# Kernel tuning notes

Measured on AMD Instinct MI355X. Metric: run time of the kernel, lower is better.

Reference implementation:

```python
import jax, jax.numpy as jnp
import numpy as np

N_NODES = 20000


def _segment_softmax(alpha, dst, num_nodes):
    # numerically-stable softmax over edges grouped by destination node
    m = jax.ops.segment_max(alpha, dst, num_segments=num_nodes)
    m = jnp.where(jnp.isfinite(m), m, 0.0)
    a = jnp.exp(alpha - m[dst])
    denom = jax.ops.segment_sum(a, dst, num_segments=num_nodes)
    return a / denom[dst]


def mgcn_conv(x, src, dst, edge_type, basis, att, weight, root, bias, num_nodes):
    # x: [N, in], basis: [B, in, out], att: [R, B], weight: [R, out=in]
    x_i = x[dst]                                   # [E, in] target feats
    x_j = x[src]                                   # [E, in] source feats
    # per-edge attention logit: sum_d x_i[d] * w_r[d] * x_j[d]
    alpha = jnp.sum(x_i * weight[edge_type] * x_j, axis=1)   # [E]
    alpha = _segment_softmax(alpha, dst, num_nodes)          # [E]
    # basis-decomposed per-edge transform: x_j @ (att_r . basis)
    t = jnp.einsum('ei,bio->ebo', x_j, basis)                # [E, B, out]
    msg = jnp.einsum('ebo,eb->eo', t, att[edge_type])        # [E, out]
    msg = msg * alpha[:, None]
    out = jax.ops.segment_sum(msg, dst, num_segments=num_nodes)  # [N, out]
    return out + x @ root + bias


def setup_inputs() -> dict:
    key = jax.random.key(0)
    ks = jax.random.split(key, 16)
    E, D, R, B, N = 32768, 128, 474, 64, N_NODES
    s = 0.05
    return {
        'entity': jnp.arange(N, dtype=jnp.int64) if jax.config.jax_enable_x64 else jnp.arange(N, dtype=jnp.int32),
        'edge_index': jax.random.randint(ks[0], (2, E), 0, N, dtype=jnp.int32),
        'edge_type': jax.random.randint(ks[1], (E,), 0, R, dtype=jnp.int32),
        'emb_table': jax.random.normal(ks[2], (N, D), dtype=jnp.float32),
        'basis1': jax.random.normal(ks[3], (B, D, D), dtype=jnp.float32) * s,
        'att1': jax.random.normal(ks[4], (R, B), dtype=jnp.float32) * s,
        'weight1': jax.random.normal(ks[5], (R, D), dtype=jnp.float32) * s,
        'root1': jax.random.normal(ks[6], (D, D), dtype=jnp.float32) * s,
        'bias1': jnp.zeros((D,), dtype=jnp.float32),
        'basis2': jax.random.normal(ks[7], (B, D, D), dtype=jnp.float32) * s,
        'att2': jax.random.normal(ks[8], (R, B), dtype=jnp.float32) * s,
        'weight2': jax.random.normal(ks[9], (R, D), dtype=jnp.float32) * s,
        'root2': jax.random.normal(ks[10], (D, D), dtype=jnp.float32) * s,
        'bias2': jnp.zeros((D,), dtype=jnp.float32),
    }


def reference(entity, edge_index, edge_type, emb_table,
              basis1, att1, weight1, root1, bias1,
              basis2, att2, weight2, root2, bias2):
    src, dst = edge_index[0], edge_index[1]   # PyG: (source j, target i)
    x = emb_table[entity]                     # embedding lookup
    h = jax.nn.relu(mgcn_conv(x, src, dst, edge_type, basis1, att1,
                              weight1, root1, bias1, N_NODES))
    # dropout is identity at inference
    out = mgcn_conv(h, src, dst, edge_type, basis2, att2,
                    weight2, root2, bias2, N_NODES)
    return out
```

## Files before the change

kernel.cpp:

```cpp
#include <hip/hip_runtime.h>
#include <hip/hip_bf16.h>

#define N_NODES 20000
#define N_EDGES 32768
#define DIM 128
#define N_REL 474
#define N_BASIS 64
#define TILE_E 64
#define WSTRIDE 264
#define LELIST 1024

#define WMIX_BLKS 128
#define ROOTT_BLK 1
#define RG1_BASE (WMIX_BLKS + ROOTT_BLK)
#define RG1_BLKS ((N_NODES + 63) / 64)
#define GATHER_BASE (RG1_BASE + RG1_BLKS)
#define PREP_GRID 1024

#define MSG_REL_BLKS (2 * N_REL)
#define MERGE_GRID 1024

typedef __bf16 bf16x8 __attribute__((ext_vector_type(8)));
typedef float f32x4 __attribute__((ext_vector_type(4)));

__device__ __forceinline__ unsigned short f2b(float f) {
    unsigned u = __float_as_uint(f);
    unsigned r = (u + 0x7FFFu + ((u >> 16) & 1u)) >> 16;
    return (unsigned short)r;
}
__device__ __forceinline__ float b2f(unsigned short s) {
    return __uint_as_float(((unsigned)s) << 16);
}
__device__ __forceinline__ __bf16 u2b(unsigned short u) {
    union { unsigned short u; __bf16 b; } c; c.u = u; return c.b;
}
__device__ __forceinline__ int4 pack8(float4 a0, float4 a1) {
    int4 v;
    v.x = (int)((unsigned)f2b(a0.x) | ((unsigned)f2b(a0.y) << 16));
    v.y = (int)((unsigned)f2b(a0.z) | ((unsigned)f2b(a0.w) << 16));
    v.z = (int)((unsigned)f2b(a1.x) | ((unsigned)f2b(a1.y) << 16));
    v.w = (int)((unsigned)f2b(a1.z) | ((unsigned)f2b(a1.w) << 16));
    return v;
}
__device__ __forceinline__ float dot2bf(unsigned a, unsigned b, float wx, float wy) {
    return b2f((unsigned short)(a & 0xFFFFu)) * wx * b2f((unsigned short)(b & 0xFFFFu))
         + b2f((unsigned short)(a >> 16)) * wy * b2f((unsigned short)(b >> 16));
}

__global__ __launch_bounds__(256) void prep_kernel(const float4* __restrict__ emb,
                                                   const int* __restrict__ entity,
                                                   ushort4* __restrict__ xb4,
                                                   float4* __restrict__ zreg, int zcount4,
                                                   const float* __restrict__ att1,
                                                   const float* __restrict__ basis1,
                                                   unsigned short* __restrict__ W1,
                                                   const float* __restrict__ att2,
                                                   const float* __restrict__ basis2,
                                                   unsigned short* __restrict__ W2,
                                                   const float* __restrict__ root1,
                                                   float* __restrict__ racc1,
                                                   const float* __restrict__ root2,
                                                   unsigned short* __restrict__ rootT2) {
    __shared__ __align__(16) unsigned short bt[64 * WSTRIDE];
    int t = threadIdx.x;
    if (blockIdx.x < WMIX_BLKS) {
        int wi = blockIdx.x;
        const float* att   = (wi >= 64) ? att2 : att1;
        const float* basis = (wi >= 64) ? basis2 : basis1;
        unsigned short* W  = (wi >= 64) ? W2 : W1;
        int io0 = (wi & 63) * 256;
#pragma unroll
        for (int p = 0; p < 16; p++) {
            int c = t + 256 * p;
            int k = c >> 6, of = c & 63;
            float4 v = *(const float4*)(basis + (size_t)k * (DIM * DIM) + io0 + of * 4);
            ushort4 s;
            s.x = f2b(v.x); s.y = f2b(v.y); s.z = f2b(v.z); s.w = f2b(v.w);
            int ofx = of ^ (((k >> 3) & 7) << 2);
            *(ushort4*)&bt[k * WSTRIDE + ofx * 4] = s;
        }
        __syncthreads();

        int w = t >> 6, l = t & 63, n = l & 15, q = l >> 4;
        bf16x8 bfr[2][4];
#pragma unroll
        for (int kb = 0; kb < 2; kb++) {
            int kbase = kb * 32 + q * 8;
            int sx = ((kb * 4 + q) & 7) << 4;
#pragma unroll
            for (int c = 0; c < 4; c++) {
                int ob = (w * 64 + c * 16 + n) ^ sx;
#pragma unroll
                for (int j = 0; j < 8; j++) bfr[kb][c][j] = u2b(bt[(kbase + j) * WSTRIDE + ob]);
            }
        }
        __syncthreads();

        int srow = t >> 2, sseg = t & 3;
#pragma unroll 1
        for (int rg = 0; rg < 8; rg++) {
            int r0 = rg * 64;
            f32x4 acc[4][4] = {};
#pragma unroll
            for (int kb = 0; kb < 2; kb++) {
                int kbase = kb * 32 + q * 8;
                bf16x8 a[4];
#pragma unroll
                for (int rt = 0; rt < 4; rt++) {
                    int rm = min(r0 + rt * 16 + n, N_REL - 1);
                    const float4* ap = (const float4*)(att + (size_t)rm * N_BASIS + kbase);
                    float4 u0 = ap[0], u1 = ap[1];
                    a[rt][0] = (__bf16)u0.x; a[rt][1] = (__bf16)u0.y;
                    a[rt][2] = (__bf16)u0.z; a[rt][3] = (__bf16)u0.w;
                    a[rt][4] = (__bf16)u1.x; a[rt][5] = (__bf16)u1.y;
                    a[rt][6] = (__bf16)u1.z; a[rt][7] = (__bf16)u1.w;
                }
#pragma unroll
                for (int c = 0; c < 4; c++) {
#pragma unroll
                    for (int rt = 0; rt < 4; rt++)
                        acc[rt][c] = __builtin_amdgcn_mfma_f32_16x16x32_bf16(a[rt], bfr[kb][c], acc[rt][c], 0, 0, 0);
                }
            }
#pragma unroll
            for (int rt = 0; rt < 4; rt++) {
#pragma unroll
                for (int c = 0; c < 4; c++) {
#pragma unroll
                    for (int g = 0; g < 4; g++)
                        bt[(rt * 16 + q * 4 + g) * WSTRIDE + w * 64 + c * 16 + n] = f2b(acc[rt][c][g]);
                }
            }
            __syncthreads();
            int rr = r0 + srow;
            if (rr < N_REL) {
                const int4* sp = (const int4*)&bt[srow * WSTRIDE];
                unsigned short* wp = W + (size_t)rr * (DIM * DIM) + io0;
#pragma unroll
                for (int ii = 0; ii < 8; ii++) {
                    int i = (ii + sseg * 2) & 7;
                    int4 v = sp[sseg * 8 + i];
                    *(int4*)(wp + sseg * 64 + i * 8) = v;
                }
            }
            __syncthreads();
        }
    } else if (blockIdx.x < RG1_BASE) {
        unsigned short* sb16 = bt;
#pragma unroll
        for (int p = 0; p < 16; p++) {
            int idx = t + 256 * p;
            int k = idx >> 5, o4 = idx & 31;
            float4 v = ((const float4*)root2)[idx];
            ushort4 s;
            s.x = f2b(v.x); s.y = f2b(v.y); s.z = f2b(v.z); s.w = f2b(v.w);
            *(ushort4*)&sb16[k * 132 + o4 * 4] = s;
        }
        __syncthreads();
        int o = t >> 1, kh = (t & 1) * 64;
#pragma unroll
        for (int i = 0; i < 16; i++) {
            int k0 = kh + i * 4;
            ushort4 s;
            s.x = sb16[(k0 + 0) * 132 + o];
            s.y = sb16[(k0 + 1) * 132 + o];
            s.z = sb16[(k0 + 2) * 132 + o];
            s.w = sb16[(k0 + 3) * 132 + o];
            *(ushort4*)&rootT2[o * DIM + k0] = s;
        }
    } else if (blockIdx.x < GATHER_BASE) {
        int n0 = (blockIdx.x - RG1_BASE) * 64;
        unsigned short* xrf = bt;
#pragma unroll
        for (int p = 0; p < 4; p++) {
            int c = t + 256 * p;
            int g = c >> 6;
            int rt = g >> 2, kb = g & 3;
            int q2 = (c >> 4) & 3, m = c & 15;
            int row = n0 + rt * 16 + m;
            int oct = kb * 4 + q2;
            int4 v = make_int4(0, 0, 0, 0);
            if (row < N_NODES) {
                const float4* sp = emb + (size_t)entity[row] * 32 + oct * 2;
                v = pack8(sp[0], sp[1]);
            }
            *(int4*)&xrf[c * 8] = v;
        }
        __syncthreads();

        int w_ = t >> 6, l = t & 63, n = l & 15, q = l >> 4;
        f32x4 acc[2][4] = {};
#pragma unroll
        for (int kb = 0; kb < 4; kb++) {
            bf16x8 a[4];
#pragma unroll
            for (int rt = 0; rt < 4; rt++) a[rt] = *(const bf16x8*)&xrf[((rt * 4 + kb) * 64 + l) * 8];
            int kbase = kb * 32 + q * 8;
#pragma unroll
            for (int c = 0; c < 2; c++) {
                int col = (w_ * 2 + c) * 16 + n;
                bf16x8 b;
#pragma unroll
                for (int j = 0; j < 8; j++) b[j] = (__bf16)root1[(kbase + j) * DIM + col];
#pragma unroll
                for (int rt = 0; rt < 4; rt++)
                    acc[c][rt] = __builtin_amdgcn_mfma_f32_16x16x32_bf16(a[rt], b, acc[c][rt], 0, 0, 0);
            }
        }
#pragma unroll
        for (int c = 0; c < 2; c++) {
            int col = (w_ * 2 + c) * 16 + n;
#pragma unroll
            for (int rt = 0; rt < 4; rt++) {
#pragma unroll
                for (int rg = 0; rg < 4; rg++) {
                    int row = n0 + rt * 16 + q * 4 + rg;
                    if (row < N_NODES)
                        racc1[(size_t)row * DIM + col] = acc[c][rt][rg];
                }
            }
        }
    } else {
        int pb = blockIdx.x - GATHER_BASE;
        int gtid = pb * 256 + t;
        int gsz = (PREP_GRID - GATHER_BASE) * 256;
        int total4 = N_NODES * DIM / 4;
        for (int i = gtid; i < total4; i += gsz) {
            int n = i >> 5, rem = i & 31;
            float4 v = emb[(size_t)entity[n] * 32 + rem];
            ushort4 s;
            s.x = f2b(v.x); s.y = f2b(v.y); s.z = f2b(v.z); s.w = f2b(v.w);
            xb4[i] = s;
        }
        float4 z = make_float4(0.f, 0.f, 0.f, 0.f);
        for (int i = gtid; i < zcount4; i += gsz) zreg[i] = z;
    }
}

__global__ __launch_bounds__(256) void msg_kernel(const unsigned short* __restrict__ xb,
                                                  const unsigned short* __restrict__ W,
                                                  const float* __restrict__ wlog,
                                                  const int* __restrict__ src,
                                                  const int* __restrict__ dst,
                                                  const int* __restrict__ etype,
                                                  float* __restrict__ den,
                                                  float* __restrict__ accm,
                                                  const unsigned short* __restrict__ rootT,
                                                  float* __restrict__ racc) {
    __shared__ __align__(16) unsigned short wt[128 * 136];
    __shared__ __align__(16) unsigned short xjf[8192];
    __shared__ __align__(16) float wf[DIM];
    __shared__ float scf[TILE_E];
    __shared__ int sdd[TILE_E];
    __shared__ int ssrc[TILE_E];
    __shared__ int elist[LELIST];
    __shared__ int lcnt;

    int t = threadIdx.x;
    if ((int)blockIdx.x < MSG_REL_BLKS) {
        int r = blockIdx.x >> 1, half = blockIdx.x & 1;
        const unsigned short* Wr = W + (size_t)r * (DIM * DIM);
        if (t == 0) lcnt = 0;
#pragma unroll
        for (int p = 0; p < 8; p++) {
            int c = t + 256 * p;
            int k = c >> 4, oct = c & 15;
            int4 v = *(const int4*)(Wr + k * DIM + oct * 8);
            int oct2 = oct ^ (((k >> 3) & 7) << 1);
            *(int4*)&wt[k * 136 + oct2 * 8] = v;
        }
        if (t < 32) ((float4*)wf)[t] = ((const float4*)(wlog + (size_t)r * DIM))[t];
        __syncthreads();

        int lane = t & 63;
        for (int it = half * 16; it < half * 16 + 16; it++) {
            int idx = it * 256 + t;
            int4 ev = ((const int4*)etype)[idx];
#pragma unroll
            for (int j = 0; j < 4; j++) {
                int etj = (j == 0) ? ev.x : (j == 1) ? ev.y : (j == 2) ? ev.z : ev.w;
                bool m = (etj == r);
                unsigned long long bal = __ballot(m);
                int tot = __popcll(bal);
                if (tot) {
                    int base = 0;
                    if (lane == 0) base = atomicAdd(&lcnt, tot);
                    base = __shfl(base, 0, 64);
                    if (m) {
                        int pre = __popcll(bal & ((1ull << lane) - 1ull));
                        int p_ = base + pre;
                        if (p_ < LELIST) elist[p_] = idx * 4 + j;
                    }
                }
            }
        }
        __syncthreads();
        int cnt = min(lcnt, LELIST);
        if (cnt == 0) return;

        int w = t >> 6, l = t & 63, n = l & 15, q = l >> 4;
        int el4 = t >> 2, l4 = t & 3;

        for (int t0 = 0; t0 < cnt; t0 += TILE_E) {
            int nE = min(TILE_E, cnt - t0);
            if (t < TILE_E) {
                if (t < nE) {
                    int e = elist[t0 + t];
                    ssrc[t] = src[e];
                    sdd[t]  = dst[e];
                } else { ssrc[t] = 0; sdd[t] = 0; }
            }
            __syncthreads();

            {
                int s_ = ssrc[el4], d_ = sdd[el4];
                const int4* xj = (const int4*)(xb + (size_t)s_ * DIM) + l4 * 4;
                const int4* xi = (const int4*)(xb + (size_t)d_ * DIM) + l4 * 4;
                const float4* wv = (const float4*)&wf[l4 * 32];
                float v = 0.f;
#pragma unroll
                for (int u = 0; u < 4; u++) {
                    int4 a = xj[u]; int4 bb = xi[u];
                    float4 w0 = wv[u * 2], w1 = wv[u * 2 + 1];
                    v += dot2bf((unsigned)a.x, (unsigned)bb.x, w0.x, w0.y)
                       + dot2bf((unsigned)a.y, (unsigned)bb.y, w0.z, w0.w)
                       + dot2bf((unsigned)a.z, (unsigned)bb.z, w1.x, w1.y)
                       + dot2bf((unsigned)a.w, (unsigned)bb.w, w1.z, w1.w);
                }
                v += __shfl_xor(v, 1, 64);
                v += __shfl_xor(v, 2, 64);
                if (l4 == 0) {
                    if (el4 < nE) {
                        float a = expf(v);
                        scf[el4] = a;
                        atomicAdd(&den[d_], a);
                    } else scf[el4] = 0.f;
                }
            }

#pragma unroll
            for (int p = 0; p < 4; p++) {
                int c = t + 256 * p;
                int g = c >> 6;
                int rt = g >> 2, kb = g & 3;
                int q2 = (c >> 4) & 3, m = c & 15;
                int e = rt * 16 + m;
                int oct = kb * 4 + q2;
                int4 v = make_int4(0, 0, 0, 0);
                if (e < nE) v = *(const int4*)(xb + (size_t)ssrc[e] * DIM + oct * 8);
                *(int4*)&xjf[c * 8] = v;
            }
            __syncthreads();

            f32x4 acc[2][4] = {};
#pragma unroll
            for (int kb = 0; kb < 4; kb++) {
                bf16x8 a[4];
#pragma unroll
                for (int rt = 0; rt < 4; rt++) a[rt] = *(const bf16x8*)&xjf[((rt * 4 + kb) * 64 + l) * 8];
                int kbase = kb * 32 + q * 8;
                int sx = ((kb * 4 + q) & 7) << 4;
#pragma unroll
                for (int c = 0; c < 2; c++) {
                    int ob = ((w * 2 + c) * 16 + n) ^ sx;
                    bf16x8 bb;
#pragma unroll
                    for (int j = 0; j < 8; j++) bb[j] = u2b(wt[(kbase + j) * 136 + ob]);
#pragma unroll
                    for (int rt = 0; rt < 4; rt++)
                        acc[c][rt] = __builtin_amdgcn_mfma_f32_16x16x32_bf16(a[rt], bb, acc[c][rt], 0, 0, 0);
                }
            }
#pragma unroll
            for (int c = 0; c < 2; c++) {
                int col = (w * 2 + c) * 16 + n;
#pragma unroll
                for (int rt = 0; rt < 4; rt++) {
#pragma unroll
                    for (int rg = 0; rg < 4; rg++) {
                        int e = rt * 16 + q * 4 + rg;
                        if (e < nE)
                            atomicAdd(&accm[(size_t)sdd[e] * DIM + col], scf[e] * acc[c][rt][rg]);
                    }
                }
            }
            __syncthreads();
        }
    } else {
        int n0 = ((int)blockIdx.x - MSG_REL_BLKS) * 64;
        unsigned short* xrf = wt;
#pragma unroll
        for (int p = 0; p < 4; p++) {
            int c = t + 256 * p;
            int g = c >> 6;
            int rt = g >> 2, kb = g & 3;
            int q2 = (c >> 4) & 3, m = c & 15;
            int row = n0 + rt * 16 + m;
            int oct = kb * 4 + q2;
            int4 v = make_int4(0, 0, 0, 0);
            if (row < N_NODES) v = *(const int4*)(xb + (size_t)row * DIM + oct * 8);
            *(int4*)&xrf[c * 8] = v;
        }
        __syncthreads();

        int w_ = t >> 6, l = t & 63, n = l & 15, q = l >> 4;
        f32x4 acc[2][4] = {};
#pragma unroll
        for (int kb = 0; kb < 4; kb++) {
            bf16x8 a[4];
#pragma unroll
            for (int rt = 0; rt < 4; rt++) a[rt] = *(const bf16x8*)&xrf[((rt * 4 + kb) * 64 + l) * 8];
            int kbase = kb * 32 + q * 8;
#pragma unroll
            for (int c = 0; c < 2; c++) {
                int col = (w_ * 2 + c) * 16 + n;
                bf16x8 bb = *(const bf16x8*)(rootT + (size_t)col * DIM + kbase);
#pragma unroll
                for (int rt = 0; rt < 4; rt++)
                    acc[c][rt] = __builtin_amdgcn_mfma_f32_16x16x32_bf16(a[rt], bb, acc[c][rt], 0, 0, 0);
            }
        }
#pragma unroll
        for (int c = 0; c < 2; c++) {
            int col = (w_ * 2 + c) * 16 + n;
#pragma unroll
            for (int rt = 0; rt < 4; rt++) {
#pragma unroll
                for (int rg = 0; rg < 4; rg++) {
                    int row = n0 + rt * 16 + q * 4 + rg;
                    if (row < N_NODES)
                        racc[(size_t)row * DIM + col] = acc[c][rt][rg];
                }
            }
        }
    }
}

__global__ __launch_bounds__(256) void merge_kernel(const float4* __restrict__ racc,
                                                    const float4* __restrict__ accm,
                                                    const float* __restrict__ den,
                                                    const float* __restrict__ bias,
                                                    float4* __restrict__ outf,
                                                    ushort4* __restrict__ outb) {
    int gtid = blockIdx.x * 256 + threadIdx.x;
    const int tot4 = N_NODES * (DIM / 4);
    for (int i = gtid; i < tot4; i += (int)gridDim.x * 256) {
        int row = i >> 5;
        int c0 = (i & 31) * 4;
        float4 rv = racc[i];
        float4 mv = accm[i];
        float4 bo = *(const float4*)&bias[c0];
        float dv = den[row];
        float inv = dv > 0.f ? 1.0f / dv : 0.f;
        float4 v;
        v.x = rv.x + bo.x + mv.x * inv;
        v.y = rv.y + bo.y + mv.y * inv;
        v.z = rv.z + bo.z + mv.z * inv;
        v.w = rv.w + bo.w + mv.w * inv;
        if (outb) {
            ushort4 s;
            s.x = f2b(fmaxf(v.x, 0.f)); s.y = f2b(fmaxf(v.y, 0.f));
            s.z = f2b(fmaxf(v.z, 0.f)); s.w = f2b(fmaxf(v.w, 0.f));
            outb[i] = s;
        } else {
            outf[i] = v;
        }
    }
}

extern "C" void kernel_launch(void* const* d_in, const int* in_sizes, int n_in,
                              void* d_out, int out_size, void* d_ws, size_t ws_size,
                              hipStream_t stream) {
    const int N = N_NODES, E = N_EDGES, R = N_REL;

    const int* entity = (const int*)d_in[0];
    const int* eidx   = (const int*)d_in[1];
    const int* src    = eidx;
    const int* dst    = eidx + E;
    const int* etype  = (const int*)d_in[2];
    const float* emb  = (const float*)d_in[3];
    const float* basis1 = (const float*)d_in[4];
    const float* att1   = (const float*)d_in[5];
    const float* w1     = (const float*)d_in[6];
    const float* root1  = (const float*)d_in[7];
    const float* bias1  = (const float*)d_in[8];
    const float* basis2 = (const float*)d_in[9];
    const float* att2   = (const float*)d_in[10];
    const float* w2     = (const float*)d_in[11];
    const float* root2  = (const float*)d_in[12];
    const float* bias2  = (const float*)d_in[13];
    float* out = (float*)d_out;

    size_t off = 0;
    auto alloc = [&](size_t bytes) -> void* {
        void* p = (char*)d_ws + off;
        off += (bytes + 255) & ~(size_t)255;
        return p;
    };
    unsigned short* W1 = (unsigned short*)alloc((size_t)R * DIM * DIM * 2);
    unsigned short* W2 = (unsigned short*)alloc((size_t)R * DIM * DIM * 2);
    unsigned short* xb = (unsigned short*)alloc((size_t)N * DIM * 2);
    unsigned short* hb = (unsigned short*)alloc((size_t)N * DIM * 2);
    float* racc1  = (float*)alloc((size_t)N * DIM * 4);
    float* racc2  = (float*)alloc((size_t)N * DIM * 4);
    float* zreg   = (float*)alloc(((size_t)2 * N + (size_t)2 * N * DIM) * 4);
    float* den1   = zreg;
    float* den2   = zreg + N;
    float* accm1  = zreg + 2 * N;
    float* accm2  = zreg + 2 * N + (size_t)N * DIM;
    unsigned short* rootT2 = (unsigned short*)alloc((size_t)DIM * DIM * 2);

    int zcount4 = (2 * N + 2 * N * DIM) / 4;

    prep_kernel<<<PREP_GRID, 256, 0, stream>>>(
        (const float4*)emb, entity, (ushort4*)xb, (float4*)zreg, zcount4,
        att1, basis1, W1, att2, basis2, W2, root1, racc1, root2, rootT2);

    msg_kernel<<<MSG_REL_BLKS, 256, 0, stream>>>(xb, W1, w1, src, dst, etype,
                                                 den1, accm1, nullptr, nullptr);
    merge_kernel<<<MERGE_GRID, 256, 0, stream>>>((const float4*)racc1, (const float4*)accm1,
                                                 den1, bias1, nullptr, (ushort4*)hb);

    msg_kernel<<<MSG_REL_BLKS + RG1_BLKS, 256, 0, stream>>>(hb, W2, w2, src, dst, etype,
                                                            den2, accm2, rootT2, racc2);
    merge_kernel<<<MERGE_GRID, 256, 0, stream>>>((const float4*)racc2, (const float4*)accm2,
                                                 den2, bias2, (float4*)out, nullptr);
}
```

Baseline: 215.3 us.

## Split relation-weight mixing across more blocks and move layer-1 root GEMM into msg kernel

The W mixing in prep is spread over 1024 blocks, one per (layer, column chunk, relation group), instead of 128 blocks that each loop over 8 relation groups. This gives more parallelism and removes the long serial tail in the prep kernel. The layer-1 root GEMM is moved out of prep and into the first msg_kernel launch, so both layers share the same path using a transposed bf16 root matrix. The cost is that each mixing block reloads and re-swizzles its basis slice into shared memory, so basis reads increase eightfold.

```diff
diff --git a/kernel.cpp b/kernel.cpp
--- a/kernel.cpp
+++ b/kernel.cpp
@@ -10,14 +10,14 @@
 #define WSTRIDE 264
 #define LELIST 1024
 
-#define WMIX_BLKS 128
-#define ROOTT_BLK 1
-#define RG1_BASE (WMIX_BLKS + ROOTT_BLK)
-#define RG1_BLKS ((N_NODES + 63) / 64)
-#define GATHER_BASE (RG1_BASE + RG1_BLKS)
-#define PREP_GRID 1024
+#define WMIX_BLKS 1024
+#define ROOTT_BLKS 2
+#define GATHER_BASE (WMIX_BLKS + ROOTT_BLKS)
+#define PREP_GRID 1664
 
 #define MSG_REL_BLKS (2 * N_REL)
+#define RG_BLKS ((N_NODES + 63) / 64)
+#define MSG_GRID (MSG_REL_BLKS + RG_BLKS)
 #define MERGE_GRID 1024
 
 typedef __bf16 bf16x8 __attribute__((ext_vector_type(8)));
@@ -33,14 +33,6 @@
 }
 __device__ __forceinline__ __bf16 u2b(unsigned short u) {
     union { unsigned short u; __bf16 b; } c; c.u = u; return c.b;
-}
-__device__ __forceinline__ int4 pack8(float4 a0, float4 a1) {
-    int4 v;
-    v.x = (int)((unsigned)f2b(a0.x) | ((unsigned)f2b(a0.y) << 16));
-    v.y = (int)((unsigned)f2b(a0.z) | ((unsigned)f2b(a0.w) << 16));
-    v.z = (int)((unsigned)f2b(a1.x) | ((unsigned)f2b(a1.y) << 16));
-    v.w = (int)((unsigned)f2b(a1.z) | ((unsigned)f2b(a1.w) << 16));
-    return v;
 }
 __device__ __forceinline__ float dot2bf(unsigned a, unsigned b, float wx, float wy) {
     return b2f((unsigned short)(a & 0xFFFFu)) * wx * b2f((unsigned short)(b & 0xFFFFu))
@@ -58,17 +50,21 @@
                                                    const float* __restrict__ basis2,
                                                    unsigned short* __restrict__ W2,
                                                    const float* __restrict__ root1,
-                                                   float* __restrict__ racc1,
+                                                   unsigned short* __restrict__ rootT1,
                                                    const float* __restrict__ root2,
                                                    unsigned short* __restrict__ rootT2) {
     __shared__ __align__(16) unsigned short bt[64 * WSTRIDE];
     int t = threadIdx.x;
     if (blockIdx.x < WMIX_BLKS) {
         int wi = blockIdx.x;
-        const float* att   = (wi >= 64) ? att2 : att1;
-        const float* basis = (wi >= 64) ? basis2 : basis1;
-        unsigned short* W  = (wi >= 64) ? W2 : W1;
-        int io0 = (wi & 63) * 256;
+        int layer = wi >> 9;
+        int cb = (wi >> 3) & 63;
+        int rg = wi & 7;
+        const float* att   = layer ? att2 : att1;
+        const float* basis = layer ? basis2 : basis1;
+        unsigned short* W  = layer ? W2 : W1;
+        int io0 = cb * 256;
+        int r0 = rg * 64;
 #pragma unroll
         for (int p = 0; p < 16; p++) {
             int c = t + 256 * p;
@@ -96,62 +92,60 @@
         }
         __syncthreads();
 
+        f32x4 acc[4][4] = {};
+#pragma unroll
+        for (int kb = 0; kb < 2; kb++) {
+            int kbase = kb * 32 + q * 8;
+            bf16x8 a[4];
+#pragma unroll
+            for (int rt = 0; rt < 4; rt++) {
+                int rm = min(r0 + rt * 16 + n, N_REL - 1);
+                const float4* ap = (const float4*)(att + (size_t)rm * N_BASIS + kbase);
+                float4 u0 = ap[0], u1 = ap[1];
+                a[rt][0] = (__bf16)u0.x; a[rt][1] = (__bf16)u0.y;
+                a[rt][2] = (__bf16)u0.z; a[rt][3] = (__bf16)u0.w;
+                a[rt][4] = (__bf16)u1.x; a[rt][5] = (__bf16)u1.y;
+                a[rt][6] = (__bf16)u1.z; a[rt][7] = (__bf16)u1.w;
+            }
+#pragma unroll
+            for (int c = 0; c < 4; c++) {
+#pragma unroll
+                for (int rt = 0; rt < 4; rt++)
+                    acc[rt][c] = __builtin_amdgcn_mfma_f32_16x16x32_bf16(a[rt], bfr[kb][c], acc[rt][c], 0, 0, 0);
+            }
+        }
+#pragma unroll
+        for (int rt = 0; rt < 4; rt++) {
+#pragma unroll
+            for (int c = 0; c < 4; c++) {
+#pragma unroll
+                for (int g = 0; g < 4; g++)
+                    bt[(rt * 16 + q * 4 + g) * WSTRIDE + w * 64 + c * 16 + n] = f2b(acc[rt][c][g]);
+            }
+        }
+        __syncthreads();
         int srow = t >> 2, sseg = t & 3;
-#pragma unroll 1
-        for (int rg = 0; rg < 8; rg++) {
-            int r0 = rg * 64;
-            f32x4 acc[4][4] = {};
-#pragma unroll
-            for (int kb = 0; kb < 2; kb++) {
-                int kbase = kb * 32 + q * 8;
-                bf16x8 a[4];
-#pragma unroll
-                for (int rt = 0; rt < 4; rt++) {
-                    int rm = min(r0 + rt * 16 + n, N_REL - 1);
-                    const float4* ap = (const float4*)(att + (size_t)rm * N_BASIS + kbase);
-                    float4 u0 = ap[0], u1 = ap[1];
-                    a[rt][0] = (__bf16)u0.x; a[rt][1] = (__bf16)u0.y;
-                    a[rt][2] = (__bf16)u0.z; a[rt][3] = (__bf16)u0.w;
-                    a[rt][4] = (__bf16)u1.x; a[rt][5] = (__bf16)u1.y;
-                    a[rt][6] = (__bf16)u1.z; a[rt][7] = (__bf16)u1.w;
-                }
-#pragma unroll
-                for (int c = 0; c < 4; c++) {
-#pragma unroll
-                    for (int rt = 0; rt < 4; rt++)
-                        acc[rt][c] = __builtin_amdgcn_mfma_f32_16x16x32_bf16(a[rt], bfr[kb][c], acc[rt][c], 0, 0, 0);
-                }
-            }
-#pragma unroll
-            for (int rt = 0; rt < 4; rt++) {
-#pragma unroll
-                for (int c = 0; c < 4; c++) {
-#pragma unroll
-                    for (int g = 0; g < 4; g++)
-                        bt[(rt * 16 + q * 4 + g) * WSTRIDE + w * 64 + c * 16 + n] = f2b(acc[rt][c][g]);
-                }
-            }
-            __syncthreads();
-            int rr = r0 + srow;
-            if (rr < N_REL) {
-                const int4* sp = (const int4*)&bt[srow * WSTRIDE];
-                unsigned short* wp = W + (size_t)rr * (DIM * DIM) + io0;
-#pragma unroll
-                for (int ii = 0; ii < 8; ii++) {
-                    int i = (ii + sseg * 2) & 7;
-                    int4 v = sp[sseg * 8 + i];
-                    *(int4*)(wp + sseg * 64 + i * 8) = v;
-                }
-            }
-            __syncthreads();
-        }
-    } else if (blockIdx.x < RG1_BASE) {
+        int rr = r0 + srow;
+        if (rr < N_REL) {
+            const int4* sp = (const int4*)&bt[srow * WSTRIDE];
+            unsigned short* wp = W + (size_t)rr * (DIM * DIM) + io0;
+#pragma unroll
+            for (int ii = 0; ii < 8; ii++) {
+                int i = (ii + sseg * 2) & 7;
+                int4 v = sp[sseg * 8 + i];
+                *(int4*)(wp + sseg * 64 + i * 8) = v;
+            }
+        }
+    } else if (blockIdx.x < GATHER_BASE) {
+        int wi2 = blockIdx.x - WMIX_BLKS;
+        const float* rm = wi2 ? root2 : root1;
+        unsigned short* rt_ = wi2 ? rootT2 : rootT1;
         unsigned short* sb16 = bt;
 #pragma unroll
         for (int p = 0; p < 16; p++) {
             int idx = t + 256 * p;
             int k = idx >> 5, o4 = idx & 31;
-            float4 v = ((const float4*)root2)[idx];
+            float4 v = ((const float4*)rm)[idx];
             ushort4 s;
             s.x = f2b(v.x); s.y = f2b(v.y); s.z = f2b(v.z); s.w = f2b(v.w);
             *(ushort4*)&sb16[k * 132 + o4 * 4] = s;
@@ -166,59 +160,7 @@
             s.y = sb16[(k0 + 1) * 132 + o];
             s.z = sb16[(k0 + 2) * 132 + o];
             s.w = sb16[(k0 + 3) * 132 + o];
-            *(ushort4*)&rootT2[o * DIM + k0] = s;
-        }
-    } else if (blockIdx.x < GATHER_BASE) {
-        int n0 = (blockIdx.x - RG1_BASE) * 64;
-        unsigned short* xrf = bt;
-#pragma unroll
-        for (int p = 0; p < 4; p++) {
-            int c = t + 256 * p;
-            int g = c >> 6;
-            int rt = g >> 2, kb = g & 3;
-            int q2 = (c >> 4) & 3, m = c & 15;
-            int row = n0 + rt * 16 + m;
-            int oct = kb * 4 + q2;
-            int4 v = make_int4(0, 0, 0, 0);
-            if (row < N_NODES) {
-                const float4* sp = emb + (size_t)entity[row] * 32 + oct * 2;
-                v = pack8(sp[0], sp[1]);
-            }
-            *(int4*)&xrf[c * 8] = v;
-        }
-        __syncthreads();
-
-        int w_ = t >> 6, l = t & 63, n = l & 15, q = l >> 4;
-        f32x4 acc[2][4] = {};
-#pragma unroll
-        for (int kb = 0; kb < 4; kb++) {
-            bf16x8 a[4];
-#pragma unroll
-            for (int rt = 0; rt < 4; rt++) a[rt] = *(const bf16x8*)&xrf[((rt * 4 + kb) * 64 + l) * 8];
-            int kbase = kb * 32 + q * 8;
-#pragma unroll
-            for (int c = 0; c < 2; c++) {
-                int col = (w_ * 2 + c) * 16 + n;
-                bf16x8 b;
-#pragma unroll
-                for (int j = 0; j < 8; j++) b[j] = (__bf16)root1[(kbase + j) * DIM + col];
-#pragma unroll
-                for (int rt = 0; rt < 4; rt++)
-                    acc[c][rt] = __builtin_amdgcn_mfma_f32_16x16x32_bf16(a[rt], b, acc[c][rt], 0, 0, 0);
-            }
-        }
-#pragma unroll
-        for (int c = 0; c < 2; c++) {
-            int col = (w_ * 2 + c) * 16 + n;
-#pragma unroll
-            for (int rt = 0; rt < 4; rt++) {
-#pragma unroll
-                for (int rg = 0; rg < 4; rg++) {
-                    int row = n0 + rt * 16 + q * 4 + rg;
-                    if (row < N_NODES)
-                        racc1[(size_t)row * DIM + col] = acc[c][rt][rg];
-                }
-            }
+            *(ushort4*)&rt_[o * DIM + k0] = s;
         }
     } else {
         int pb = blockIdx.x - GATHER_BASE;
@@ -508,21 +450,22 @@
     float* den2   = zreg + N;
     float* accm1  = zreg + 2 * N;
     float* accm2  = zreg + 2 * N + (size_t)N * DIM;
+    unsigned short* rootT1 = (unsigned short*)alloc((size_t)DIM * DIM * 2);
     unsigned short* rootT2 = (unsigned short*)alloc((size_t)DIM * DIM * 2);
 
     int zcount4 = (2 * N + 2 * N * DIM) / 4;
 
     prep_kernel<<<PREP_GRID, 256, 0, stream>>>(
         (const float4*)emb, entity, (ushort4*)xb, (float4*)zreg, zcount4,
-        att1, basis1, W1, att2, basis2, W2, root1, racc1, root2, rootT2);
-
-    msg_kernel<<<MSG_REL_BLKS, 256, 0, stream>>>(xb, W1, w1, src, dst, etype,
-                                                 den1, accm1, nullptr, nullptr);
+        att1, basis1, W1, att2, basis2, W2, root1, rootT1, root2, rootT2);
+
+    msg_kernel<<<MSG_GRID, 256, 0, stream>>>(xb, W1, w1, src, dst, etype,
+                                             den1, accm1, rootT1, racc1);
     merge_kernel<<<MERGE_GRID, 256, 0, stream>>>((const float4*)racc1, (const float4*)accm1,
                                                  den1, bias1, nullptr, (ushort4*)hb);
 
-    msg_kernel<<<MSG_REL_BLKS + RG1_BLKS, 256, 0, stream>>>(hb, W2, w2, src, dst, etype,
-                                                            den2, accm2, rootT2, racc2);
+    msg_kernel<<<MSG_GRID, 256, 0, stream>>>(hb, W2, w2, src, dst, etype,
+                                             den2, accm2, rootT2, racc2);
     merge_kernel<<<MERGE_GRID, 256, 0, stream>>>((const float4*)racc2, (const float4*)accm2,
                                                  den2, bias2, (float4*)out, nullptr);
 }
```

Measured after the change: 209.2 us. 2.9% less time.
